# Kernel tuning notes

Measured on AMD Instinct MI355X. Metric: run time of the kernel, lower is better.

The kernel has to match this reference:

```python
import jax, jax.numpy as jnp
import numpy as np

NUM_EMB = 1_000_000
EMB_DIM = 64
ATT_DIM = 64
NUM_BAGS = 16384
BAG_LEN = 50  # total indices = NUM_BAGS * BAG_LEN = 819200


def setup_inputs() -> dict:
    key = jax.random.key(0)
    k1, k2, k3, k4, k5 = jax.random.split(key, 5)
    N = NUM_BAGS * BAG_LEN
    input_ = jax.random.randint(k1, (N,), 0, NUM_EMB, dtype=jnp.int64)
    # CSR indptr: fixed-size bags of BAG_LEN (sorted, starts at 0)
    offsets = (jnp.arange(NUM_BAGS, dtype=jnp.int64) * BAG_LEN)
    emb_weight = jax.random.normal(k2, (NUM_EMB, EMB_DIM), dtype=jnp.float32) * 0.05
    proj_w = jax.random.normal(k3, (ATT_DIM, EMB_DIM), dtype=jnp.float32) * (1.0 / np.sqrt(EMB_DIM))
    proj_b = jax.random.normal(k4, (ATT_DIM,), dtype=jnp.float32) * 0.01
    att_h = jax.random.normal(k5, (ATT_DIM,), dtype=jnp.float32) * 0.01
    return {"input_": input_, "offsets": offsets, "emb_weight": emb_weight,
            "proj_w": proj_w, "proj_b": proj_b, "att_h": att_h}


def reference(input_, offsets, emb_weight, proj_w, proj_b, att_h):
    N = input_.shape[0]
    B = offsets.shape[0]
    # Gather embedding rows once; reused for both attention logits and pooling.
    att_emb = emb_weight[input_]                                  # [N, D]
    # logits = tanh(emb @ W^T + b) . att_h
    att = jnp.einsum('na,a->n', jnp.tanh(att_emb @ proj_w.T + proj_b), att_h)  # [N]
    # segment id for each index from CSR indptr (repeat_interleave equivalent)
    seg = jnp.searchsorted(offsets, jnp.arange(N), side='right') - 1           # [N]
    # stable segment softmax over ragged bags
    m = jax.ops.segment_max(att, seg, num_segments=B)            # [B]
    e = jnp.exp(att - m[seg])                                    # [N]
    s = jax.ops.segment_sum(e, seg, num_segments=B)              # [B]
    w = e / s[seg]                                               # [N]
    # attention-weighted sum pooling (embedding_bag with per_sample_weights)
    return jax.ops.segment_sum(w[:, None] * att_emb, seg, num_segments=B)     # [B, D]
```

## Files before the change

kernel.cpp:

```cpp
#include <hip/hip_runtime.h>
#include <hip/hip_bf16.h>
#include <math.h>

#define EMB_DIM 64
#define MAXL    64

typedef __attribute__((ext_vector_type(8))) short  bf16x8;
typedef __attribute__((ext_vector_type(8))) ushort u16x8;
typedef __attribute__((ext_vector_type(4))) float  f32x4;

static __device__ __forceinline__ ushort f2bf(float x) {
    __hip_bfloat16 h = __float2bfloat16(x);
    return __builtin_bit_cast(ushort, h);
}
static __device__ __forceinline__ float bf2f(ushort u) {
    return __uint_as_float(((unsigned)u) << 16);
}
static __device__ __forceinline__ bf16x8 pack8(float4 a, float4 b) {
    bf16x8 r;
    r[0] = (short)f2bf(a.x); r[1] = (short)f2bf(a.y);
    r[2] = (short)f2bf(a.z); r[3] = (short)f2bf(a.w);
    r[4] = (short)f2bf(b.x); r[5] = (short)f2bf(b.y);
    r[6] = (short)f2bf(b.z); r[7] = (short)f2bf(b.w);
    return r;
}

__global__ void convert_w_perm(const float* __restrict__ proj_w,
                               ushort* __restrict__ w_perm) {
    const int g = blockIdx.x * 256 + threadIdx.x;
    if (g >= 64 * 64) return;
    const int e    = g & 7;
    const int lane = (g >> 3) & 63;
    const int blk  = g >> 9;
    const int s    = blk & 1;
    const int t    = blk >> 1;
    const int c    = lane & 15;
    const int rg   = lane >> 4;
    const int jj   = e >> 2;
    const int m    = e & 3;
    const int a    = 16 * t + c;
    const int k    = 16 * (2 * s + jj) + 4 * rg + m;
    w_perm[g] = f2bf(proj_w[a * EMB_DIM + k]);
}

__global__ __launch_bounds__(256, 4)
void pooled_attn_coal(const int* __restrict__ input_,
                      const int* __restrict__ offsets,
                      const float* __restrict__ emb,
                      const ushort* __restrict__ w_perm,
                      const float* __restrict__ proj_b,
                      const float* __restrict__ att_h,
                      float* __restrict__ out,
                      int n_bags, int n_total)
{
    __shared__ ushort Wl[512 * 8];
    __shared__ float  Att[4][MAXL];

    const int tid  = threadIdx.x;
    const int lane = tid & 63;
    const int wv   = tid >> 6;
    const int c    = lane & 15;
    const int rg   = lane >> 4;

    #pragma unroll
    for (int k = tid; k < 512; k += 256)
        *(u16x8*)&Wl[(size_t)k * 8] = *(const u16x8*)&w_perm[(size_t)k * 8];

    float bbias[4], hval[4];
    #pragma unroll
    for (int t = 0; t < 4; ++t) {
        bbias[t] = proj_b[c + 16 * t];
        hval[t]  = att_h[c + 16 * t];
    }
    __syncthreads();

    const int b = blockIdx.x * 4 + wv;
    if (b >= n_bags) return;
    float* att = Att[wv];

    const int s0 = offsets[b];
    const int e1 = (b + 1 < n_bags) ? offsets[b + 1] : n_total;
    int L = e1 - s0; L = L < 0 ? 0 : (L > MAXL ? MAXL : L);
    const int myidx = (lane < L) ? input_[s0 + lane] : 0;

    float4 st[16];
    #pragma unroll
    for (int ti = 0; ti < 4; ++ti) {
        const int row  = 16 * ti + c;
        const int ridx = __shfl(myidx, row, 64);
        const float4* rp = (const float4*)(emb + (size_t)ridx * EMB_DIM);
        #pragma unroll
        for (int j = 0; j < 4; ++j)
            st[ti * 4 + j] = rp[4 * j + rg];
    }

    bf16x8 ea[4][2];
    ea[0][0] = pack8(st[0],  st[1]);  ea[0][1] = pack8(st[2],  st[3]);
    ea[1][0] = pack8(st[4],  st[5]);  ea[1][1] = pack8(st[6],  st[7]);

    #pragma unroll
    for (int ch = 0; ch < 4; ++ch) {
        if (ch == 2) {
            ea[2][0] = pack8(st[8],  st[9]);  ea[2][1] = pack8(st[10], st[11]);
            ea[3][0] = pack8(st[12], st[13]); ea[3][1] = pack8(st[14], st[15]);
        }
        f32x4 acc[4];
        #pragma unroll
        for (int t = 0; t < 4; ++t) acc[t] = (f32x4){0.f, 0.f, 0.f, 0.f};
        #pragma unroll
        for (int s = 0; s < 2; ++s) {
            #pragma unroll
            for (int t = 0; t < 4; ++t) {
                bf16x8 bbf = *(const bf16x8*)&Wl[((t * 2 + s) * 64 + lane) * 8];
                acc[t] = __builtin_amdgcn_mfma_f32_16x16x32_bf16(ea[ch][s], bbf, acc[t], 0, 0, 0);
            }
        }
        float vatt[4] = {0.f, 0.f, 0.f, 0.f};
        #pragma unroll
        for (int t = 0; t < 4; ++t) {
            #pragma unroll
            for (int r = 0; r < 4; ++r) {
                const float z = acc[t][r] + bbias[t];
                const float u = z * z;
                float p = fmaf(-0.05396825397f, u, 0.1333333333f);
                p = fmaf(p, u, -0.3333333333f);
                p = fmaf(p, u, 1.0f);
                vatt[r] = fmaf(z * p, hval[t], vatt[r]);
            }
        }
        #pragma unroll
        for (int r = 0; r < 4; ++r) {
            float v = vatt[r];
            v += __shfl_xor(v, 1, 16);
            v += __shfl_xor(v, 2, 16);
            v += __shfl_xor(v, 4, 16);
            v += __shfl_xor(v, 8, 16);
            vatt[r] = v;
        }
        if (c == 0) {
            f32x4 v4 = {vatt[0], vatt[1], vatt[2], vatt[3]};
            *(f32x4*)&att[16 * ch + 4 * rg] = v4;
        }
    }

    const float av = (lane < L) ? att[lane] : -INFINITY;
    float m = av;
    #pragma unroll
    for (int o = 32; o; o >>= 1) m = fmaxf(m, __shfl_xor(m, o, 64));
    const float ee = (lane < L) ? __expf(av - m) : 0.0f;
    float ssum = ee;
    #pragma unroll
    for (int o = 32; o; o >>= 1) ssum += __shfl_xor(ssum, o, 64);
    const float wt = ee * (1.0f / ssum);

    float pool[16];
    #pragma unroll
    for (int k = 0; k < 16; ++k) pool[k] = 0.f;
    #pragma unroll
    for (int ch = 0; ch < 4; ++ch) {
        const float wr = __shfl(wt, 16 * ch + c, 64);
        #pragma unroll
        for (int s = 0; s < 2; ++s)
            #pragma unroll
            for (int j = 0; j < 8; ++j)
                pool[s * 8 + j] = fmaf(wr, bf2f((ushort)ea[ch][s][j]), pool[s * 8 + j]);
    }
    #pragma unroll
    for (int o = 1; o < 16; o <<= 1) {
        #pragma unroll
        for (int k = 0; k < 16; ++k) pool[k] += __shfl_xor(pool[k], o, 16);
    }
    if (c == 0) {
        float* op = out + (size_t)b * EMB_DIM;
        *(float4*)&op[4 * rg]      = make_float4(pool[0],  pool[1],  pool[2],  pool[3]);
        *(float4*)&op[16 + 4 * rg] = make_float4(pool[4],  pool[5],  pool[6],  pool[7]);
        *(float4*)&op[32 + 4 * rg] = make_float4(pool[8],  pool[9],  pool[10], pool[11]);
        *(float4*)&op[48 + 4 * rg] = make_float4(pool[12], pool[13], pool[14], pool[15]);
    }
}

extern "C" void kernel_launch(void* const* d_in, const int* in_sizes, int n_in,
                              void* d_out, int out_size, void* d_ws, size_t ws_size,
                              hipStream_t stream) {
    const int*   input_  = (const int*)d_in[0];
    const int*   offsets = (const int*)d_in[1];
    const float* emb     = (const float*)d_in[2];
    const float* proj_w  = (const float*)d_in[3];
    const float* proj_b  = (const float*)d_in[4];
    const float* att_h   = (const float*)d_in[5];
    float* out = (float*)d_out;

    const int N = in_sizes[0];
    const int B = in_sizes[1];

    ushort* w_perm = (ushort*)d_ws;

    convert_w_perm<<<(EMB_DIM * EMB_DIM + 255) / 256, 256, 0, stream>>>(proj_w, w_perm);
    pooled_attn_coal<<<(B + 3) / 4, 256, 0, stream>>>(
        input_, offsets, emb, w_perm, proj_b, att_h, out, B, N);
}
```

Measured before the change: 52.12 us.

## Split each bag across two waves to cut register pressure and raise occupancy

Each bag is now handled by two wavefronts, each gathering and projecting 32 of the bag's rows, so the per-thread staging array halves. The launch bound goes from 4 to 5 blocks per CU and gathers are issued before the weight load into shared memory to overlap latency. Attention logits and partial pooled sums are exchanged through shared memory with extra __syncthreads, and one wave writes the combined output. The extra block barriers, shared-memory traffic and doubled grid size are the costs traded against higher occupancy for the latency-bound gather.

```diff
diff --git a/kernel.cpp b/kernel.cpp
--- a/kernel.cpp
+++ b/kernel.cpp
@@ -43,24 +43,49 @@
     w_perm[g] = f2bf(proj_w[a * EMB_DIM + k]);
 }
 
-__global__ __launch_bounds__(256, 4)
-void pooled_attn_coal(const int* __restrict__ input_,
-                      const int* __restrict__ offsets,
-                      const float* __restrict__ emb,
-                      const ushort* __restrict__ w_perm,
-                      const float* __restrict__ proj_b,
-                      const float* __restrict__ att_h,
-                      float* __restrict__ out,
-                      int n_bags, int n_total)
+__global__ __launch_bounds__(256, 5)
+void pooled_attn_occ(const int* __restrict__ input_,
+                     const int* __restrict__ offsets,
+                     const float* __restrict__ emb,
+                     const ushort* __restrict__ w_perm,
+                     const float* __restrict__ proj_b,
+                     const float* __restrict__ att_h,
+                     float* __restrict__ out,
+                     int n_bags, int n_total)
 {
     __shared__ ushort Wl[512 * 8];
-    __shared__ float  Att[4][MAXL];
+    __shared__ float  Att[2][MAXL];
+    __shared__ float  Pp[2][2][EMB_DIM];
 
     const int tid  = threadIdx.x;
     const int lane = tid & 63;
     const int wv   = tid >> 6;
+    const int ww   = wv & 1;
+    const int bb   = wv >> 1;
     const int c    = lane & 15;
     const int rg   = lane >> 4;
+
+    const int b  = blockIdx.x * 2 + bb;
+    const bool ok = (b < n_bags);
+
+    int L = 0, s0 = 0;
+    if (ok) {
+        s0 = offsets[b];
+        const int e1 = (b + 1 < n_bags) ? offsets[b + 1] : n_total;
+        L = e1 - s0; L = L < 0 ? 0 : (L > MAXL ? MAXL : L);
+    }
+    const int myidx = (lane < L) ? input_[s0 + lane] : 0;
+
+    float4 st[8];
+    #pragma unroll
+    for (int th = 0; th < 2; ++th) {
+        const int row  = 32 * ww + 16 * th + c;
+        const int ridx = __shfl(myidx, row, 64);
+        const float4* rp = (const float4*)(emb + (size_t)ridx * EMB_DIM);
+        #pragma unroll
+        for (int j = 0; j < 4; ++j)
+            st[th * 4 + j] = rp[4 * j + rg];
+    }
 
     #pragma unroll
     for (int k = tid; k < 512; k += 256)
@@ -74,36 +99,15 @@
     }
     __syncthreads();
 
-    const int b = blockIdx.x * 4 + wv;
-    if (b >= n_bags) return;
-    float* att = Att[wv];
-
-    const int s0 = offsets[b];
-    const int e1 = (b + 1 < n_bags) ? offsets[b + 1] : n_total;
-    int L = e1 - s0; L = L < 0 ? 0 : (L > MAXL ? MAXL : L);
-    const int myidx = (lane < L) ? input_[s0 + lane] : 0;
-
-    float4 st[16];
-    #pragma unroll
-    for (int ti = 0; ti < 4; ++ti) {
-        const int row  = 16 * ti + c;
-        const int ridx = __shfl(myidx, row, 64);
-        const float4* rp = (const float4*)(emb + (size_t)ridx * EMB_DIM);
-        #pragma unroll
-        for (int j = 0; j < 4; ++j)
-            st[ti * 4 + j] = rp[4 * j + rg];
-    }
-
-    bf16x8 ea[4][2];
-    ea[0][0] = pack8(st[0],  st[1]);  ea[0][1] = pack8(st[2],  st[3]);
-    ea[1][0] = pack8(st[4],  st[5]);  ea[1][1] = pack8(st[6],  st[7]);
-
-    #pragma unroll
-    for (int ch = 0; ch < 4; ++ch) {
-        if (ch == 2) {
-            ea[2][0] = pack8(st[8],  st[9]);  ea[2][1] = pack8(st[10], st[11]);
-            ea[3][0] = pack8(st[12], st[13]); ea[3][1] = pack8(st[14], st[15]);
-        }
+    bf16x8 ea[2][2];
+    #pragma unroll
+    for (int th = 0; th < 2; ++th) {
+        ea[th][0] = pack8(st[th * 4 + 0], st[th * 4 + 1]);
+        ea[th][1] = pack8(st[th * 4 + 2], st[th * 4 + 3]);
+    }
+
+    #pragma unroll
+    for (int th = 0; th < 2; ++th) {
         f32x4 acc[4];
         #pragma unroll
         for (int t = 0; t < 4; ++t) acc[t] = (f32x4){0.f, 0.f, 0.f, 0.f};
@@ -112,7 +116,7 @@
             #pragma unroll
             for (int t = 0; t < 4; ++t) {
                 bf16x8 bbf = *(const bf16x8*)&Wl[((t * 2 + s) * 64 + lane) * 8];
-                acc[t] = __builtin_amdgcn_mfma_f32_16x16x32_bf16(ea[ch][s], bbf, acc[t], 0, 0, 0);
+                acc[t] = __builtin_amdgcn_mfma_f32_16x16x32_bf16(ea[th][s], bbf, acc[t], 0, 0, 0);
             }
         }
         float vatt[4] = {0.f, 0.f, 0.f, 0.f};
@@ -139,11 +143,12 @@
         }
         if (c == 0) {
             f32x4 v4 = {vatt[0], vatt[1], vatt[2], vatt[3]};
-            *(f32x4*)&att[16 * ch + 4 * rg] = v4;
-        }
-    }
-
-    const float av = (lane < L) ? att[lane] : -INFINITY;
+            *(f32x4*)&Att[bb][32 * ww + 16 * th + 4 * rg] = v4;
+        }
+    }
+    __syncthreads();
+
+    const float av = (lane < L) ? Att[bb][lane] : -INFINITY;
     float m = av;
     #pragma unroll
     for (int o = 32; o; o >>= 1) m = fmaxf(m, __shfl_xor(m, o, 64));
@@ -157,13 +162,13 @@
     #pragma unroll
     for (int k = 0; k < 16; ++k) pool[k] = 0.f;
     #pragma unroll
-    for (int ch = 0; ch < 4; ++ch) {
-        const float wr = __shfl(wt, 16 * ch + c, 64);
+    for (int th = 0; th < 2; ++th) {
+        const float wr = __shfl(wt, 32 * ww + 16 * th + c, 64);
         #pragma unroll
         for (int s = 0; s < 2; ++s)
             #pragma unroll
             for (int j = 0; j < 8; ++j)
-                pool[s * 8 + j] = fmaf(wr, bf2f((ushort)ea[ch][s][j]), pool[s * 8 + j]);
+                pool[s * 8 + j] = fmaf(wr, bf2f((ushort)ea[th][s][j]), pool[s * 8 + j]);
     }
     #pragma unroll
     for (int o = 1; o < 16; o <<= 1) {
@@ -171,12 +176,15 @@
         for (int k = 0; k < 16; ++k) pool[k] += __shfl_xor(pool[k], o, 16);
     }
     if (c == 0) {
-        float* op = out + (size_t)b * EMB_DIM;
-        *(float4*)&op[4 * rg]      = make_float4(pool[0],  pool[1],  pool[2],  pool[3]);
-        *(float4*)&op[16 + 4 * rg] = make_float4(pool[4],  pool[5],  pool[6],  pool[7]);
-        *(float4*)&op[32 + 4 * rg] = make_float4(pool[8],  pool[9],  pool[10], pool[11]);
-        *(float4*)&op[48 + 4 * rg] = make_float4(pool[12], pool[13], pool[14], pool[15]);
-    }
+        #pragma unroll
+        for (int q = 0; q < 4; ++q)
+            *(f32x4*)&Pp[bb][ww][16 * q + 4 * rg] =
+                (f32x4){pool[q * 4 + 0], pool[q * 4 + 1], pool[q * 4 + 2], pool[q * 4 + 3]};
+    }
+    __syncthreads();
+
+    if (ww == 0 && ok)
+        out[(size_t)b * EMB_DIM + lane] = Pp[bb][0][lane] + Pp[bb][1][lane];
 }
 
 extern "C" void kernel_launch(void* const* d_in, const int* in_sizes, int n_in,
@@ -196,6 +204,6 @@
     ushort* w_perm = (ushort*)d_ws;
 
     convert_w_perm<<<(EMB_DIM * EMB_DIM + 255) / 256, 256, 0, stream>>>(proj_w, w_perm);
-    pooled_attn_coal<<<(B + 3) / 4, 256, 0, stream>>>(
+    pooled_attn_occ<<<(B + 1) / 2, 256, 0, stream>>>(
         input_, offsets, emb, w_perm, proj_b, att_h, out, B, N);
 }
```

Result: slower. 66.24 us (+27.1%).
